# Kernel optimization log

Measured on AMD Instinct MI355X. Metric: run time of the kernel, lower is better.

Reference implementation:

```python
import jax, jax.numpy as jnp
import numpy as np

B, C, H, W = 2, 192, 128, 128
HEADS = 4
M = 128          # num_tokens
RD = 10          # reducted_dim
GS = 256         # category_size
TDF = 16         # dim_ffn_td
HID = 4 * C      # mlp hidden (768)
HIDT = HID + TDF # 784 after concat with token-dict features
KS = 5


def _ln(x, g, b):
    mu = x.mean(-1, keepdims=True)
    var = ((x - mu) ** 2).mean(-1, keepdims=True)
    return (x - mu) / jnp.sqrt(var + 1e-5) * g + b


def _gelu(x):
    return jax.nn.gelu(x, approximate=False)  # torch nn.GELU default = exact erf


def setup_inputs() -> dict:
    key = jax.random.key(0)
    ks = jax.random.split(key, 16)
    s = 0.02
    inp = {
        "x": jax.random.normal(ks[0], (B, C, H, W), jnp.float32),
        "x_size": H,
        "td": jax.random.normal(ks[1], (M, C), jnp.float32),
        "g1": jnp.ones((C,)), "b1": jnp.zeros((C,)),
        "g2": jnp.ones((C,)), "b2": jnp.zeros((C,)),
        "g3": jnp.ones((C,)), "b3": jnp.zeros((C,)),
        "wq_w": jax.random.normal(ks[2], (C, RD)) * s, "wq_b": jnp.zeros((RD,)),
        "wk_w": jax.random.normal(ks[3], (C, RD)) * s, "wk_b": jnp.zeros((RD,)),
        "wv_w": jax.random.normal(ks[4], (C, C)) * s, "wv_b": jnp.zeros((C,)),
        "ca_scale": jnp.ones((1,)),
        "wqkv_w": jax.random.normal(ks[5], (C, 3 * C)) * s, "wqkv_b": jnp.zeros((3 * C,)),
        "proj_w": jax.random.normal(ks[6], (C, C)) * s, "proj_b": jnp.zeros((C,)),
        "fc_td_w": jax.random.normal(ks[7], (C, TDF)) * s, "fc_td_b": jnp.zeros((TDF,)),
        "fc1_w": jax.random.normal(ks[8], (C, HID)) * s, "fc1_b": jnp.zeros((HID,)),
        "dw_w": jax.random.normal(ks[9], (HIDT, 1, KS, KS)) * s, "dw_b": jnp.zeros((HIDT,)),
        "fc2_w": jax.random.normal(ks[10], (HIDT, C)) * s, "fc2_b": jnp.zeros((C,)),
    }
    return inp


def reference(x, x_size, td, g1, b1, g2, b2, g3, b3, wq_w, wq_b, wk_w, wk_b,
              wv_w, wv_b, ca_scale, wqkv_w, wqkv_b, proj_w, proj_b,
              fc_td_w, fc_td_b, fc1_w, fc1_b, dw_w, dw_b, fc2_w, fc2_b):
    b, c, h, w = x.shape
    n = h * w
    xs = x.reshape(b, c, n).transpose(0, 2, 1)          # [b,n,c] patch_embed
    shortcut = xs
    xn = _ln(xs, g1, b1)                                # norm1

    # ---- ATD_CA: L2-normalized cross-attention to token dict ----
    q = xn @ wq_w + wq_b                                # [b,n,rd]
    k = td @ wk_w + wk_b                                # [m,rd]
    v = td @ wv_w + wv_b                                # [m,c]
    qn = q / jnp.maximum(jnp.linalg.norm(q, axis=-1, keepdims=True), 1e-12)
    kn = k / jnp.maximum(jnp.linalg.norm(k, axis=-1, keepdims=True), 1e-12)
    sim = jnp.einsum('bnr,mr->bnm', qn, kn)
    scale = 1.0 + jnp.clip(ca_scale, 0.0, 3.0) * np.log(M)
    sim = jax.nn.softmax(sim * scale, axis=-1)          # [b,n,m]
    x_atd = jnp.einsum('bnm,mc->bnc', sim, v)
    tk_id = jnp.argmax(sim, axis=-1)                    # [b,n] int

    # ---- AC_MSA: category-sorted grouped self-attention ----
    qkv = xn @ wqkv_w + wqkv_b                          # [b,n,3c]
    sort_idx = jnp.argsort(tk_id, axis=-1)              # [b,n]
    inv_idx = jnp.argsort(sort_idx, axis=-1)            # index_reverse
    shuf = jnp.take_along_axis(qkv, sort_idx[:, :, None], axis=1)
    gs = min(n, GS)
    ng = (n + gs - 1) // gs
    pad_n = ng * gs - n
    pad = jnp.flip(shuf[:, n - pad_n:n, :], axis=1)
    padded = jnp.concatenate([shuf, pad], axis=1)       # [b, ng*gs, 3c]
    hd = c // HEADS
    y = padded.reshape(b, ng, gs, 3, HEADS, hd)
    y = jnp.transpose(y, (3, 0, 1, 4, 2, 5))            # [3,b,ng,H,gs,hd]
    q2, k2, v2 = y[0], y[1], y[2]
    attn = jnp.einsum('bghqd,bghkd->bghqk', q2, k2) * (hd ** -0.5)
    attn = jax.nn.softmax(attn, axis=-1)
    o = jnp.einsum('bghqk,bghkd->bghqd', attn, v2)
    o = jnp.transpose(o, (0, 1, 3, 2, 4)).reshape(b, ng * gs, c)[:, :n, :]
    o = jnp.take_along_axis(o, inv_idx[:, :, None], axis=1)
    x_aca = o @ proj_w + proj_b

    # ---- token-dict features gathered per token ----
    td_feat = td @ fc_td_w + fc_td_b                    # [m,tdf]
    x_td = jnp.take(td_feat, tk_id, axis=0)             # [b,n,tdf]

    # ---- ConvFFN_td ----
    xn2 = _ln(xs, g2, b2)
    h1 = _gelu(xn2 @ fc1_w + fc1_b)                     # [b,n,hid]
    hcat = jnp.concatenate([h1, x_td], axis=-1)         # [b,n,hidt]
    img = hcat.transpose(0, 2, 1).reshape(b, HIDT, h, w)
    conv = jax.lax.conv_general_dilated(
        img, dw_w, window_strides=(1, 1), padding=((KS // 2, KS // 2),) * 2,
        dimension_numbers=('NCHW', 'OIHW', 'NCHW'), feature_group_count=HIDT)
    conv = _gelu(conv + dw_b[None, :, None, None])
    conv = conv.reshape(b, HIDT, n).transpose(0, 2, 1)
    x_ffn = (hcat + conv) @ fc2_w + fc2_b
    x_ffn = _ln(x_ffn, g3, b3)                          # norm3

    out = shortcut + x_atd + x_aca + x_ffn
    return out.transpose(0, 2, 1).reshape(b, c, h, w)
```

## Files before the change

kernel.cpp:

```cpp
#include <hip/hip_runtime.h>
#include <hip/hip_bf16.h>
#include <math.h>

using bf16 = __hip_bfloat16;

static constexpr int B = 2, C = 192, Hh = 128, Ww = 128, N = Hh * Ww;
static constexpr int M = 128, RD = 10, GS = 256, NG = N / GS;
static constexpr int HEADS = 4, HD = C / HEADS;
static constexpr int TDF = 16, HID = 4 * C, HIDT = HID + TDF;
static constexpr int TC3 = 3 * C;
static constexpr float LOG_M = 4.852030263919617f;
static constexpr float ATT_SCALE = 0.14433756729740643f;

typedef __attribute__((ext_vector_type(8))) short bf16x8;
typedef __attribute__((ext_vector_type(4))) float f32x4;

__device__ __forceinline__ float b2f(bf16 v) { return __bfloat162float(v); }
__device__ __forceinline__ bf16 f2b(float v) { return __float2bfloat16(v); }
__device__ __forceinline__ float bits2f(unsigned short u) { return __uint_as_float(((unsigned)u) << 16); }
__device__ __forceinline__ unsigned short f2bits(float f) {
    union { bf16 h; unsigned short u; } cv; cv.h = f2b(f); return cv.u;
}
__device__ __forceinline__ float gelu_exact(float v) {
    return 0.5f * v * (1.0f + erff(v * 0.70710678118654752f));
}

__global__ void __launch_bounds__(256) k_wtrans(const float* in, bf16* out, int K, int Nn) {
    __shared__ float T[64][65];
    int n0 = blockIdx.x * 64, k0 = blockIdx.y * 64;
    int tid = threadIdx.x;
    for (int e = tid; e < 4096; e += 256) {
        int kk = e >> 6, nn = e & 63;
        if (k0 + kk < K) T[kk][nn] = in[(size_t)(k0 + kk) * Nn + n0 + nn];
    }
    __syncthreads();
    for (int e = tid; e < 4096; e += 256) {
        int nn = e >> 6, kk = e & 63;
        if (k0 + kk < K) out[(size_t)(n0 + nn) * K + k0 + kk] = f2b(T[kk][nn]);
    }
}

__global__ void k_precompute(const float* td, const float* wk_w, const float* wk_b,
                             const float* wv_w, const float* wv_b,
                             const float* fc_td_w, const float* fc_td_b,
                             float* kn, bf16* vvT, float* tdf) {
    int m = blockIdx.x;
    int lane = threadIdx.x;
    __shared__ float trow[C];
    for (int ch = lane; ch < C; ch += 64) trow[ch] = td[m * C + ch];
    __syncthreads();
    __shared__ float ks[RD];
    __shared__ float inv_s;
    if (lane < RD) {
        float s = wk_b[lane];
        for (int ch = 0; ch < C; ++ch) s += trow[ch] * wk_w[ch * RD + lane];
        ks[lane] = s;
    }
    __syncthreads();
    if (lane == 0) {
        float ss = 0.f;
        for (int r = 0; r < RD; ++r) ss += ks[r] * ks[r];
        inv_s = 1.0f / fmaxf(sqrtf(ss), 1e-12f);
    }
    __syncthreads();
    if (lane < RD) kn[m * RD + lane] = ks[lane] * inv_s;
    for (int c0 = 0; c0 < 3; ++c0) {
        int co = lane + 64 * c0;
        float s = wv_b[co];
        for (int ch = 0; ch < C; ++ch) s += trow[ch] * wv_w[ch * C + co];
        vvT[(size_t)co * M + m] = f2b(s);
    }
    if (lane < TDF) {
        float s = fc_td_b[lane];
        for (int ch = 0; ch < C; ++ch) s += trow[ch] * fc_td_w[ch * TDF + lane];
        tdf[m * TDF + lane] = s;
    }
}

__global__ void __launch_bounds__(256) k_ln(const float* x, const float* g1, const float* b1,
                                            const float* g2, const float* b2v,
                                            bf16* xn1, bf16* xn2, float* xn32, float* acc) {
    __shared__ float Xs[64 * 193];
    __shared__ float mu_s[64], rs_s[64];
    int tid = threadIdx.x;
    int m0 = blockIdx.x * 64;
    int b = m0 / N, i0 = m0 % N;
    for (int e = tid; e < 192 * 64; e += 256) {
        int ch = e >> 6, ii = e & 63;
        Xs[ii * 193 + ch] = x[((size_t)b * C + ch) * N + i0 + ii];
    }
    __syncthreads();
    {
        int tok = tid >> 2, part = tid & 3;
        float s = 0.f, ss = 0.f;
        for (int ch = part * 48; ch < part * 48 + 48; ++ch) {
            float v = Xs[tok * 193 + ch]; s += v; ss += v * v;
        }
        s += __shfl_xor(s, 1); ss += __shfl_xor(ss, 1);
        s += __shfl_xor(s, 2); ss += __shfl_xor(ss, 2);
        if (part == 0) {
            float mu = s / C;
            mu_s[tok] = mu;
            rs_s[tok] = rsqrtf(ss / C - mu * mu + 1e-5f);
        }
    }
    __syncthreads();
    for (int e = tid; e < 64 * 192; e += 256) {
        int ii = e / 192, ch = e % 192;
        float v = Xs[ii * 193 + ch];
        float xn = (v - mu_s[ii]) * rs_s[ii];
        size_t g = (size_t)(m0 + ii);
        xn1[g * C + ch] = f2b(xn * g1[ch] + b1[ch]);
        xn2[g * C + ch] = f2b(xn * g2[ch] + b2v[ch]);
        xn32[g * C + ch] = xn;
        acc[g * C + ch] = v;
    }
}

__global__ void __launch_bounds__(256) k_atdca(const float* xn32, const float* g1, const float* b1,
                        const float* wq_w, const float* wq_b, const float* ca_scale,
                        const float* kn, bf16* p_buf, int* tk_id) {
    int t0 = blockIdx.x * 4;
    int w = threadIdx.x >> 6, lane = threadIdx.x & 63;
    int g = t0 + w;
    float xn[3];
    #pragma unroll
    for (int k = 0; k < 3; ++k) {
        int ch = lane + 64 * k;
        xn[k] = xn32[(size_t)g * C + ch] * g1[ch] + b1[ch];
    }
    float q[RD];
    #pragma unroll
    for (int r = 0; r < RD; ++r) {
        float p = 0.f;
        #pragma unroll
        for (int k = 0; k < 3; ++k) { int ch = lane + 64 * k; p += xn[k] * wq_w[ch * RD + r]; }
        for (int mk = 32; mk >= 1; mk >>= 1) p += __shfl_xor(p, mk);
        q[r] = p + wq_b[r];
    }
    float ssn = 0.f;
    #pragma unroll
    for (int r = 0; r < RD; ++r) ssn += q[r] * q[r];
    float invq = 1.0f / fmaxf(sqrtf(ssn), 1e-12f);
    float s0 = 0.f, s1 = 0.f;
    #pragma unroll
    for (int r = 0; r < RD; ++r) {
        float qr = q[r] * invq;
        s0 += qr * kn[lane * RD + r];
        s1 += qr * kn[(lane + 64) * RD + r];
    }
    float mv; int mi;
    if (s1 > s0) { mv = s1; mi = lane + 64; } else { mv = s0; mi = lane; }
    for (int mk = 32; mk >= 1; mk >>= 1) {
        float ov = __shfl_xor(mv, mk); int oi = __shfl_xor(mi, mk);
        if (ov > mv || (ov == mv && oi < mi)) { mv = ov; mi = oi; }
    }
    float cs = ca_scale[0]; cs = fminf(fmaxf(cs, 0.0f), 3.0f);
    float scale = 1.0f + cs * LOG_M;
    float e0 = expf((s0 - mv) * scale), e1 = expf((s1 - mv) * scale);
    float sum = e0 + e1;
    for (int mk = 32; mk >= 1; mk >>= 1) sum += __shfl_xor(sum, mk);
    float invs = 1.0f / sum;
    p_buf[(size_t)g * M + lane] = f2b(e0 * invs);
    p_buf[(size_t)g * M + lane + 64] = f2b(e1 * invs);
    if (lane == 0) tk_id[g] = mi;
}

__global__ void __launch_bounds__(256) k_pv(const bf16* p_buf, const bf16* vvT, float* acc) {
    __shared__ __align__(16) short As[64 * 136];
    __shared__ __align__(16) short Bs[64 * 136];
    int tid = threadIdx.x;
    int m0 = blockIdx.x * 64;
    int n0 = blockIdx.y * 64;
    for (int e = tid; e < 64 * 16; e += 256) {
        int m = e >> 4, kc = (e & 15) * 8;
        *(uint4*)&As[m * 136 + kc] = *(const uint4*)(p_buf + (size_t)(m0 + m) * M + kc);
    }
    for (int e = tid; e < 64 * 16; e += 256) {
        int n = e >> 4, kc = (e & 15) * 8;
        *(uint4*)&Bs[n * 136 + kc] = *(const uint4*)(vvT + (size_t)(n0 + n) * M + kc);
    }
    __syncthreads();
    int w = tid >> 6, lane = tid & 63;
    int wm = (w >> 1) * 32, wn = (w & 1) * 32;
    int lr = lane & 15, lk = (lane >> 4) * 8;
    f32x4 acc00 = {0.f,0.f,0.f,0.f}, acc01 = acc00, acc10 = acc00, acc11 = acc00;
    #pragma unroll
    for (int ks = 0; ks < 4; ++ks) {
        int k0 = ks * 32 + lk;
        bf16x8 a0 = *(bf16x8*)&As[(wm + lr) * 136 + k0];
        bf16x8 a1 = *(bf16x8*)&As[(wm + 16 + lr) * 136 + k0];
        bf16x8 b0 = *(bf16x8*)&Bs[(wn + lr) * 136 + k0];
        bf16x8 b1 = *(bf16x8*)&Bs[(wn + 16 + lr) * 136 + k0];
        acc00 = __builtin_amdgcn_mfma_f32_16x16x32_bf16(a0, b0, acc00, 0, 0, 0);
        acc01 = __builtin_amdgcn_mfma_f32_16x16x32_bf16(a0, b1, acc01, 0, 0, 0);
        acc10 = __builtin_amdgcn_mfma_f32_16x16x32_bf16(a1, b0, acc10, 0, 0, 0);
        acc11 = __builtin_amdgcn_mfma_f32_16x16x32_bf16(a1, b1, acc11, 0, 0, 0);
    }
    int rbase = (lane >> 4) * 4;
    f32x4 accs[2][2] = {{acc00, acc01}, {acc10, acc11}};
    #pragma unroll
    for (int mt = 0; mt < 2; ++mt) {
        #pragma unroll
        for (int nt = 0; nt < 2; ++nt) {
            int co = n0 + wn + nt * 16 + lr;
            #pragma unroll
            for (int r = 0; r < 4; ++r) {
                int tok = m0 + wm + mt * 16 + rbase + r;
                acc[(size_t)tok * C + co] += accs[mt][nt][r];
            }
        }
    }
}

template<int OUTLD, int MODE>
__global__ void __launch_bounds__(256) k_gemm_big(const bf16* Abuf, const bf16* Wt, const float* bias,
                                                  bf16* outb, float* outf) {
    __shared__ __align__(16) unsigned short As[128 * 104];
    __shared__ __align__(16) unsigned short Bs[96 * 104];
    int tid = threadIdx.x;
    int m0 = blockIdx.x * 128, n0 = blockIdx.y * 96;
    int w = tid >> 6, lane = tid & 63;
    int wm = (w >> 1) * 64, wn = (w & 1) * 48;
    int lr = lane & 15, g8 = lane >> 4;
    f32x4 acc[4][3];
    #pragma unroll
    for (int mt = 0; mt < 4; ++mt)
        #pragma unroll
        for (int nt = 0; nt < 3; ++nt) acc[mt][nt] = (f32x4){0.f,0.f,0.f,0.f};
    for (int kc = 0; kc < 2; ++kc) {
        int kb = kc * 96;
        __syncthreads();
        for (int e = tid; e < 128 * 12; e += 256) {
            int m = e / 12, blk = e % 12;
            *(uint4*)&As[m * 104 + blk * 8] = *(const uint4*)(Abuf + (size_t)(m0 + m) * C + kb + blk * 8);
        }
        for (int e = tid; e < 96 * 12; e += 256) {
            int n = e / 12, blk = e % 12;
            *(uint4*)&Bs[n * 104 + blk * 8] = *(const uint4*)(Wt + (size_t)(n0 + n) * C + kb + blk * 8);
        }
        __syncthreads();
        #pragma unroll
        for (int ks = 0; ks < 3; ++ks) {
            int blk = ks * 4 + g8;
            bf16x8 a[4];
            bf16x8 bfr[3];
            #pragma unroll
            for (int mt = 0; mt < 4; ++mt) a[mt] = *(bf16x8*)&As[(wm + mt * 16 + lr) * 104 + blk * 8];
            #pragma unroll
            for (int nt = 0; nt < 3; ++nt) bfr[nt] = *(bf16x8*)&Bs[(wn + nt * 16 + lr) * 104 + blk * 8];
            #pragma unroll
            for (int mt = 0; mt < 4; ++mt)
                #pragma unroll
                for (int nt = 0; nt < 3; ++nt)
                    acc[mt][nt] = __builtin_amdgcn_mfma_f32_16x16x32_bf16(a[mt], bfr[nt], acc[mt][nt], 0, 0, 0);
        }
    }
    #pragma unroll
    for (int nt = 0; nt < 3; ++nt) {
        int co = n0 + wn + nt * 16 + lr;
        float bv = bias[co];
        #pragma unroll
        for (int mt = 0; mt < 4; ++mt) {
            #pragma unroll
            for (int r = 0; r < 4; ++r) {
                int tok = m0 + wm + mt * 16 + g8 * 4 + r;
                float v = acc[mt][nt][r] + bv;
                if (MODE == 0) outb[(size_t)tok * OUTLD + co] = f2b(v);
                else if (MODE == 1) outb[(size_t)tok * OUTLD + co] = f2b(gelu_exact(v));
                else outf[(size_t)tok * OUTLD + co] += v;
            }
        }
    }
}

__global__ void k_sort_count(const int* tk_id, int* chunk_cnt) {
    int c = blockIdx.x, b = blockIdx.y;
    int tid = threadIdx.x;
    __shared__ int cnt[M];
    cnt[tid] = 0;
    __syncthreads();
    atomicAdd(&cnt[tk_id[b * N + c * 128 + tid]], 1);
    __syncthreads();
    chunk_cnt[(b * 128 + c) * M + tid] = cnt[tid];
}

__global__ void k_sort_scan(int* chunk_cnt) {
    int b = blockIdx.x;
    int k = threadIdx.x;
    int tot = 0;
    for (int c = 0; c < 128; ++c) tot += chunk_cnt[(b * 128 + c) * M + k];
    __shared__ int totals[M];
    __shared__ int base[M];
    totals[k] = tot;
    __syncthreads();
    if (k == 0) {
        int run = 0;
        for (int kk = 0; kk < M; ++kk) { base[kk] = run; run += totals[kk]; }
    }
    __syncthreads();
    int run = base[k];
    for (int c = 0; c < 128; ++c) {
        int v = chunk_cnt[(b * 128 + c) * M + k];
        chunk_cnt[(b * 128 + c) * M + k] = run;
        run += v;
    }
}

__global__ void k_sort_scatter(const int* tk_id, const int* chunk_cnt, int* sort_idx) {
    int c = blockIdx.x, b = blockIdx.y;
    int k = threadIdx.x;
    __shared__ int keys[128];
    keys[k] = tk_id[b * N + c * 128 + k];
    __syncthreads();
    int off = chunk_cnt[(b * 128 + c) * M + k];
    for (int j = 0; j < 128; ++j) {
        if (keys[j] == k) sort_idx[b * N + off++] = c * 128 + j;
    }
}

__global__ void __launch_bounds__(256) k_attn_mfma(const bf16* qkv, const int* sort_idx, bf16* o_buf) {
    int g = blockIdx.x, h = blockIdx.y, b = blockIdx.z;
    __shared__ int sidx[GS];
    __shared__ __align__(16) unsigned short Kl[256 * 64];
    __shared__ __align__(16) unsigned short Vt[48 * 256];
    __shared__ __align__(16) unsigned short Pl[4][64 * 32];
    int tid = threadIdx.x;
    sidx[tid] = sort_idx[b * N + g * GS + tid];
    __syncthreads();
    {
        int row = tid;
        int srow = sidx[row];
        size_t kb = ((size_t)(b * N + srow)) * TC3 + C + h * HD;
        size_t vb = ((size_t)(b * N + srow)) * TC3 + 2 * C + h * HD;
        #pragma unroll
        for (int db = 0; db < 6; ++db) {
            uint4 kv = *(const uint4*)(qkv + kb + db * 8);
            *(uint4*)&Kl[row * 64 + ((db ^ (row & 7)) * 8)] = kv;
            uint4 vv4 = *(const uint4*)(qkv + vb + db * 8);
            unsigned short* vu = (unsigned short*)&vv4;
            #pragma unroll
            for (int j = 0; j < 8; ++j) {
                int d = db * 8 + j;
                Vt[d * 256 + (((row >> 3) ^ (d & 7)) * 8) + (row & 7)] = vu[j];
            }
        }
        uint4 z = {0u,0u,0u,0u};
        *(uint4*)&Kl[row * 64 + ((6 ^ (row & 7)) * 8)] = z;
        *(uint4*)&Kl[row * 64 + ((7 ^ (row & 7)) * 8)] = z;
    }
    __syncthreads();
    int w = tid >> 6, l = tid & 63;
    int lq = l & 15, g8 = l >> 4;
    bf16x8 qf[4][2];
    #pragma unroll
    for (int qt = 0; qt < 4; ++qt) {
        int qrow = sidx[w * 64 + qt * 16 + lq];
        size_t qb = ((size_t)(b * N + qrow)) * TC3 + h * HD;
        qf[qt][0] = *(const bf16x8*)(qkv + qb + g8 * 8);
        int d1 = 32 + g8 * 8;
        if (d1 < HD) qf[qt][1] = *(const bf16x8*)(qkv + qb + d1);
        else { uint4 z = {0u,0u,0u,0u}; qf[qt][1] = *(bf16x8*)&z; }
    }
    float mrun[4], lrun[4];
    f32x4 Oa[4][3];
    #pragma unroll
    for (int qt = 0; qt < 4; ++qt) {
        mrun[qt] = -1e30f; lrun[qt] = 0.f;
        #pragma unroll
        for (int dt = 0; dt < 3; ++dt) Oa[qt][dt] = (f32x4){0.f,0.f,0.f,0.f};
    }
    unsigned short* Pw = &Pl[w][0];
    for (int ck = 0; ck < 8; ++ck) {
        int kbase = ck * 32;
        bf16x8 kf[2][2];
        #pragma unroll
        for (int kt = 0; kt < 2; ++kt) {
            int key = kbase + kt * 16 + lq;
            #pragma unroll
            for (int ks = 0; ks < 2; ++ks)
                kf[kt][ks] = *(bf16x8*)&Kl[key * 64 + (((ks * 4 + g8) ^ (key & 7)) * 8)];
        }
        bf16x8 vf[3];
        #pragma unroll
        for (int dt = 0; dt < 3; ++dt) {
            int d = dt * 16 + lq;
            vf[dt] = *(bf16x8*)&Vt[d * 256 + ((((kbase >> 3) + g8) ^ (d & 7)) * 8)];
        }
        #pragma unroll
        for (int qt = 0; qt < 4; ++qt) {
            f32x4 s0 = {0.f,0.f,0.f,0.f}, s1 = s0;
            s0 = __builtin_amdgcn_mfma_f32_16x16x32_bf16(kf[0][0], qf[qt][0], s0, 0, 0, 0);
            s0 = __builtin_amdgcn_mfma_f32_16x16x32_bf16(kf[0][1], qf[qt][1], s0, 0, 0, 0);
            s1 = __builtin_amdgcn_mfma_f32_16x16x32_bf16(kf[1][0], qf[qt][0], s1, 0, 0, 0);
            s1 = __builtin_amdgcn_mfma_f32_16x16x32_bf16(kf[1][1], qf[qt][1], s1, 0, 0, 0);
            float sv0[4], sv1[4];
            float cmax = -1e30f;
            #pragma unroll
            for (int r = 0; r < 4; ++r) {
                sv0[r] = s0[r] * ATT_SCALE; sv1[r] = s1[r] * ATT_SCALE;
                cmax = fmaxf(cmax, fmaxf(sv0[r], sv1[r]));
            }
            cmax = fmaxf(cmax, __shfl_xor(cmax, 16));
            cmax = fmaxf(cmax, __shfl_xor(cmax, 32));
            float mnew = fmaxf(mrun[qt], cmax);
            float sf = expf(mrun[qt] - mnew);
            float p0[4], p1[4], csum = 0.f;
            #pragma unroll
            for (int r = 0; r < 4; ++r) {
                p0[r] = expf(sv0[r] - mnew); p1[r] = expf(sv1[r] - mnew);
                csum += p0[r] + p1[r];
            }
            csum += __shfl_xor(csum, 16);
            csum += __shfl_xor(csum, 32);
            lrun[qt] = lrun[qt] * sf + csum;
            mrun[qt] = mnew;
            int q = qt * 16 + lq;
            {
                unsigned short pw[4];
                #pragma unroll
                for (int r = 0; r < 4; ++r) pw[r] = f2bits(p0[r]);
                int slot = g8;
                int addr = q * 32 + (((slot >> 1) ^ (q & 3)) * 8) + (slot & 1) * 4;
                *(uint2*)&Pw[addr] = *(uint2*)pw;
                #pragma unroll
                for (int r = 0; r < 4; ++r) pw[r] = f2bits(p1[r]);
                slot = 4 + g8;
                addr = q * 32 + (((slot >> 1) ^ (q & 3)) * 8) + (slot & 1) * 4;
                *(uint2*)&Pw[addr] = *(uint2*)pw;
            }
            float sfr[4];
            #pragma unroll
            for (int r = 0; r < 4; ++r) sfr[r] = __shfl(sf, 4 * g8 + r);
            #pragma unroll
            for (int dt = 0; dt < 3; ++dt)
                #pragma unroll
                for (int r = 0; r < 4; ++r) Oa[qt][dt][r] *= sfr[r];
            bf16x8 pa = *(bf16x8*)&Pw[q * 32 + ((g8 ^ (lq & 3)) * 8)];
            #pragma unroll
            for (int dt = 0; dt < 3; ++dt)
                Oa[qt][dt] = __builtin_amdgcn_mfma_f32_16x16x32_bf16(pa, vf[dt], Oa[qt][dt], 0, 0, 0);
        }
    }
    #pragma unroll
    for (int qt = 0; qt < 4; ++qt) {
        float invq = 1.0f / lrun[qt];
        float invr[4];
        #pragma unroll
        for (int r = 0; r < 4; ++r) invr[r] = __shfl(invq, 4 * g8 + r);
        #pragma unroll
        for (int r = 0; r < 4; ++r) {
            int grow = sidx[w * 64 + qt * 16 + 4 * g8 + r];
            size_t obase = ((size_t)(b * N + grow)) * C + h * HD;
            #pragma unroll
            for (int dt = 0; dt < 3; ++dt)
                o_buf[obase + dt * 16 + lq] = f2b(Oa[qt][dt][r] * invr[r]);
        }
    }
}

__global__ void k_tdfill(const int* tk_id, const float* tdf, bf16* hcat) {
    int idx = blockIdx.x * 256 + threadIdx.x;
    if (idx >= B * N * TDF) return;
    int tok = idx >> 4, f = idx & 15;
    hcat[(size_t)tok * HIDT + HID + f] = f2b(tdf[tk_id[tok] * TDF + f]);
}

__global__ void __launch_bounds__(256) k_conv(const bf16* hcat, const float* dw_w, const float* dw_b,
                                              bf16* convsum) {
    int st = blockIdx.x;
    int c16 = blockIdx.y;
    int b = blockIdx.z;
    int tx0 = (st & 7) * 16, ty0 = (st >> 3) * 16;
    int tid = threadIdx.x;
    __shared__ __align__(16) float Hf[20 * 81 * 4];
    __shared__ __align__(16) float Wf[25 * 16];
    __shared__ float Wb[16];
    for (int e = tid; e < 400; e += 256) {
        int tap = e >> 4, ch = e & 15;
        Wf[e] = dw_w[(size_t)(c16 * 16 + ch) * 25 + tap];
    }
    if (tid < 16) Wb[tid] = dw_b[c16 * 16 + tid];
    for (int e = tid; e < 800; e += 256) {
        int pos = e >> 1, sc = e & 1;
        int py = pos / 20, px = pos % 20;
        int gy = ty0 + py - 2, gx = tx0 + px - 2;
        uint4 v = {0u, 0u, 0u, 0u};
        if (gy >= 0 && gy < Hh && gx >= 0 && gx < Ww)
            v = *(const uint4*)(hcat + ((size_t)b * N + gy * Ww + gx) * HIDT + c16 * 16 + sc * 8);
        unsigned short* u = (unsigned short*)&v;
        float4 f0 = { bits2f(u[0]), bits2f(u[1]), bits2f(u[2]), bits2f(u[3]) };
        float4 f1 = { bits2f(u[4]), bits2f(u[5]), bits2f(u[6]), bits2f(u[7]) };
        int base = (py * 81 + px * 4 + sc * 2) * 4;
        *(float4*)&Hf[base] = f0;
        *(float4*)&Hf[base + 4] = f1;
    }
    __syncthreads();
    int cc = tid & 1, lx = (tid >> 1) & 7, ly = tid >> 4;
    float acc[2][8] = {};
    #pragma unroll 1
    for (int ky = 0; ky < 5; ++ky) {
        int py = ly + ky;
        float4 w[5][2];
        #pragma unroll
        for (int kx = 0; kx < 5; ++kx) {
            w[kx][0] = *(float4*)&Wf[(ky * 5 + kx) * 16 + cc * 8];
            w[kx][1] = *(float4*)&Wf[(ky * 5 + kx) * 16 + cc * 8 + 4];
        }
        #pragma unroll
        for (int c = 0; c < 6; ++c) {
            int px = 2 * lx + c;
            int base = (py * 81 + px * 4 + cc * 2) * 4;
            float4 f0 = *(float4*)&Hf[base];
            float4 f1 = *(float4*)&Hf[base + 4];
            float f[8] = { f0.x, f0.y, f0.z, f0.w, f1.x, f1.y, f1.z, f1.w };
            #pragma unroll
            for (int kx = 0; kx < 5; ++kx) {
                int ox = c - kx;
                if (ox >= 0 && ox < 2) {
                    const float* wp = (const float*)&w[kx][0];
                    #pragma unroll
                    for (int j = 0; j < 8; ++j) acc[ox][j] += f[j] * wp[j];
                }
            }
        }
    }
    int gy = ty0 + ly;
    #pragma unroll
    for (int ox = 0; ox < 2; ++ox) {
        int px = 2 * lx + ox + 2, py = ly + 2;
        int base = (py * 81 + px * 4 + cc * 2) * 4;
        float4 f0 = *(float4*)&Hf[base];
        float4 f1 = *(float4*)&Hf[base + 4];
        float cf[8] = { f0.x, f0.y, f0.z, f0.w, f1.x, f1.y, f1.z, f1.w };
        unsigned short ow[8];
        #pragma unroll
        for (int j = 0; j < 8; ++j)
            ow[j] = f2bits(cf[j] + gelu_exact(acc[ox][j] + Wb[cc * 8 + j]));
        int gx = tx0 + 2 * lx + ox;
        *(uint4*)(convsum + ((size_t)b * N + gy * Ww + gx) * HIDT + c16 * 16 + cc * 8) = *(uint4*)ow;
    }
}

__global__ void __launch_bounds__(256) k_fc2ln(const bf16* convsum, const bf16* Wt,
                                               const float* bias, const float* g3, const float* b3,
                                               const float* accres, float* out) {
    __shared__ __align__(16) char smem[65536];
    unsigned short* AsB = (unsigned short*)smem;
    unsigned short* BsB = (unsigned short*)(smem + 16384);
    float* Ot = (float*)smem;
    int tid = threadIdx.x;
    int m0 = blockIdx.x * 64;
    int w = tid >> 6, lane = tid & 63;
    int lr = lane & 15, g8 = lane >> 4;
    f32x4 acc[12];
    #pragma unroll
    for (int nt = 0; nt < 12; ++nt) acc[nt] = (f32x4){0.f, 0.f, 0.f, 0.f};

    auto stage = [&](int d, int kc) {
        int kb = kc * 64;
        unsigned short* As = AsB + d * 4096;
        unsigned short* Bs = BsB + d * 12288;
        for (int e = tid; e < 512; e += 256) {
            int m = e >> 3, k8 = (e & 7) * 8;
            uint4 v = {0u,0u,0u,0u};
            if (kb + k8 < HIDT) v = *(const uint4*)(convsum + (size_t)(m0 + m) * HIDT + kb + k8);
            *(uint4*)&As[m * 64 + (((e & 7) ^ (m & 7)) * 8)] = v;
        }
        for (int e = tid; e < 1536; e += 256) {
            int n = e >> 3, k8 = (e & 7) * 8;
            uint4 v = {0u,0u,0u,0u};
            if (kb + k8 < HIDT) v = *(const uint4*)(Wt + (size_t)n * HIDT + kb + k8);
            *(uint4*)&Bs[n * 64 + (((e & 7) ^ (n & 7)) * 8)] = v;
        }
    };
    stage(0, 0);
    int cur = 0;
    for (int kc = 0; kc < 13; ++kc) {
        __syncthreads();
        if (kc + 1 < 13) stage(cur ^ 1, kc + 1);
        unsigned short* As = AsB + cur * 4096;
        unsigned short* Bs = BsB + cur * 12288;
        #pragma unroll
        for (int ks = 0; ks < 2; ++ks) {
            int kg = ks * 4 + g8;
            int arow = w * 16 + lr;
            bf16x8 a = *(bf16x8*)&As[arow * 64 + ((kg ^ (arow & 7)) * 8)];
            #pragma unroll
            for (int nt = 0; nt < 12; ++nt) {
                int nrow = nt * 16 + lr;
                bf16x8 bfr = *(bf16x8*)&Bs[nrow * 64 + ((kg ^ (nrow & 7)) * 8)];
                acc[nt] = __builtin_amdgcn_mfma_f32_16x16x32_bf16(a, bfr, acc[nt], 0, 0, 0);
            }
        }
        cur ^= 1;
    }
    #pragma unroll
    for (int nt = 0; nt < 12; ++nt) {
        float bv = bias[nt * 16 + lr];
        #pragma unroll
        for (int r = 0; r < 4; ++r) acc[nt][r] += bv;
    }
    float mu_r[4], rs_r[4];
    #pragma unroll
    for (int r = 0; r < 4; ++r) {
        float s = 0.f, ss = 0.f;
        #pragma unroll
        for (int nt = 0; nt < 12; ++nt) { float v = acc[nt][r]; s += v; ss += v * v; }
        s += __shfl_xor(s, 1); ss += __shfl_xor(ss, 1);
        s += __shfl_xor(s, 2); ss += __shfl_xor(ss, 2);
        s += __shfl_xor(s, 4); ss += __shfl_xor(ss, 4);
        s += __shfl_xor(s, 8); ss += __shfl_xor(ss, 8);
        mu_r[r] = s / C;
        rs_r[r] = rsqrtf(ss / C - mu_r[r] * mu_r[r] + 1e-5f);
    }
    int bb = m0 / N, i0 = m0 % N;
    for (int h = 0; h < 2; ++h) {
        __syncthreads();
        #pragma unroll
        for (int ntl = 0; ntl < 6; ++ntl) {
            int nt = h * 6 + ntl;
            int c = nt * 16 + lr;
            float g3v = g3[c], b3v = b3[c];
            #pragma unroll
            for (int r = 0; r < 4; ++r) {
                int tok = m0 + w * 16 + g8 * 4 + r;
                float o = accres[(size_t)tok * C + c] + (acc[nt][r] - mu_r[r]) * rs_r[r] * g3v + b3v;
                Ot[(ntl * 16 + lr) * 68 + w * 16 + g8 * 4 + r] = o;
            }
        }
        __syncthreads();
        for (int e = tid; e < 96 * 16; e += 256) {
            int row = e >> 4, q4 = e & 15;
            int c = h * 96 + row;
            float4 v = *(float4*)&Ot[row * 68 + q4 * 4];
            *(float4*)(out + ((size_t)(bb * C + c)) * N + i0 + q4 * 4) = v;
        }
    }
}

__global__ void k_sentinel(float* out, int nelem) {
    int i = blockIdx.x * blockDim.x + threadIdx.x;
    if (i < nelem) out[i] = 1234.0f;
}

extern "C" void kernel_launch(void* const* d_in, const int* in_sizes, int n_in,
                              void* d_out, int out_size, void* d_ws, size_t ws_size,
                              hipStream_t stream) {
    const float* x        = (const float*)d_in[0];
    const float* td       = (const float*)d_in[2];
    const float* g1       = (const float*)d_in[3];
    const float* b1       = (const float*)d_in[4];
    const float* g2       = (const float*)d_in[5];
    const float* b2v      = (const float*)d_in[6];
    const float* g3       = (const float*)d_in[7];
    const float* b3       = (const float*)d_in[8];
    const float* wq_w     = (const float*)d_in[9];
    const float* wq_b     = (const float*)d_in[10];
    const float* wk_w     = (const float*)d_in[11];
    const float* wk_b     = (const float*)d_in[12];
    const float* wv_w     = (const float*)d_in[13];
    const float* wv_b     = (const float*)d_in[14];
    const float* ca_scale = (const float*)d_in[15];
    const float* wqkv_w   = (const float*)d_in[16];
    const float* wqkv_b   = (const float*)d_in[17];
    const float* proj_w   = (const float*)d_in[18];
    const float* proj_b   = (const float*)d_in[19];
    const float* fc_td_w  = (const float*)d_in[20];
    const float* fc_td_b  = (const float*)d_in[21];
    const float* fc1_w    = (const float*)d_in[22];
    const float* fc1_b    = (const float*)d_in[23];
    const float* dw_w     = (const float*)d_in[24];
    const float* dw_b     = (const float*)d_in[25];
    const float* fc2_w    = (const float*)d_in[26];
    const float* fc2_b    = (const float*)d_in[27];
    float* out = (float*)d_out;

    char* ws = (char*)d_ws;
    size_t off = 0;
    auto alloc = [&](size_t bytes) { size_t o = off; off += (bytes + 255) & ~(size_t)255; return o; };
    size_t o_xn1   = alloc((size_t)B * N * C * 2);
    size_t o_xn2   = alloc((size_t)B * N * C * 2);
    size_t o_xn32  = alloc((size_t)B * N * C * 4);
    size_t o_acc   = alloc((size_t)B * N * C * 4);
    size_t o_qkv   = alloc((size_t)B * N * TC3 * 2);
    size_t o_obuf  = alloc((size_t)B * N * C * 2);
    size_t o_hcat  = alloc((size_t)B * N * HIDT * 2);
    size_t o_conv  = alloc((size_t)B * N * HIDT * 2);
    size_t o_kn    = alloc((size_t)M * RD * 4);
    size_t o_vvT   = alloc((size_t)C * M * 2);
    size_t o_tdf   = alloc((size_t)M * TDF * 4);
    size_t o_tk    = alloc((size_t)B * N * 4);
    size_t o_sidx  = alloc((size_t)B * N * 4);
    size_t o_ccnt  = alloc((size_t)B * 128 * M * 4);
    size_t o_pbuf  = alloc((size_t)B * N * M * 2);
    size_t o_wqkvT = alloc((size_t)TC3 * C * 2);
    size_t o_projT = alloc((size_t)C * C * 2);
    size_t o_fc1T  = alloc((size_t)HID * C * 2);
    size_t o_fc2T  = alloc((size_t)C * HIDT * 2);

    if (ws_size < off) {
        k_sentinel<<<(out_size + 255) / 256, 256, 0, stream>>>(out, out_size);
        return;
    }

    bf16*  xn1     = (bf16*)(ws + o_xn1);
    bf16*  xn2     = (bf16*)(ws + o_xn2);
    float* xn32    = (float*)(ws + o_xn32);
    float* acc     = (float*)(ws + o_acc);
    bf16*  qkv     = (bf16*)(ws + o_qkv);
    bf16*  o_bufp  = (bf16*)(ws + o_obuf);
    bf16*  hcat    = (bf16*)(ws + o_hcat);
    bf16*  convsum = (bf16*)(ws + o_conv);
    float* kn      = (float*)(ws + o_kn);
    bf16*  vvT     = (bf16*)(ws + o_vvT);
    float* tdf     = (float*)(ws + o_tdf);
    int*   tk_id   = (int*)(ws + o_tk);
    int*   sidx    = (int*)(ws + o_sidx);
    int*   ccnt    = (int*)(ws + o_ccnt);
    bf16*  p_buf   = (bf16*)(ws + o_pbuf);
    bf16*  wqkvT   = (bf16*)(ws + o_wqkvT);
    bf16*  projT   = (bf16*)(ws + o_projT);
    bf16*  fc1T    = (bf16*)(ws + o_fc1T);
    bf16*  fc2T    = (bf16*)(ws + o_fc2T);

    k_wtrans<<<dim3(TC3 / 64, C / 64), 256, 0, stream>>>(wqkv_w, wqkvT, C, TC3);
    k_wtrans<<<dim3(C / 64, C / 64), 256, 0, stream>>>(proj_w, projT, C, C);
    k_wtrans<<<dim3(HID / 64, C / 64), 256, 0, stream>>>(fc1_w, fc1T, C, HID);
    k_wtrans<<<dim3(C / 64, (HIDT + 63) / 64), 256, 0, stream>>>(fc2_w, fc2T, HIDT, C);

    k_precompute<<<M, 64, 0, stream>>>(td, wk_w, wk_b, wv_w, wv_b, fc_td_w, fc_td_b, kn, vvT, tdf);
    k_ln<<<B * N / 64, 256, 0, stream>>>(x, g1, b1, g2, b2v, xn1, xn2, xn32, acc);
    k_atdca<<<B * N / 4, 256, 0, stream>>>(xn32, g1, b1, wq_w, wq_b, ca_scale, kn, p_buf, tk_id);
    k_pv<<<dim3(B * N / 64, C / 64), 256, 0, stream>>>(p_buf, vvT, acc);
    k_gemm_big<TC3, 0><<<dim3(B * N / 128, TC3 / 96), 256, 0, stream>>>(
        xn1, wqkvT, wqkv_b, qkv, nullptr);
    k_sort_count<<<dim3(128, B), 128, 0, stream>>>(tk_id, ccnt);
    k_sort_scan<<<B, 128, 0, stream>>>(ccnt);
    k_sort_scatter<<<dim3(128, B), 128, 0, stream>>>(tk_id, ccnt, sidx);
    k_attn_mfma<<<dim3(NG, HEADS, B), 256, 0, stream>>>(qkv, sidx, o_bufp);
    k_gemm_big<C, 2><<<dim3(B * N / 128, C / 96), 256, 0, stream>>>(
        o_bufp, projT, proj_b, nullptr, acc);
    k_gemm_big<HIDT, 1><<<dim3(B * N / 128, HID / 96), 256, 0, stream>>>(
        xn2, fc1T, fc1_b, hcat, nullptr);
    k_tdfill<<<(B * N * TDF + 255) / 256, 256, 0, stream>>>(tk_id, tdf, hcat);
    k_conv<<<dim3(64, 49, B), 256, 0, stream>>>(hcat, dw_w, dw_b, convsum);
    k_fc2ln<<<B * N / 64, 256, 0, stream>>>(convsum, fc2T, fc2_b, g3, b3, acc, out);
}
```

Before: 399.4 us.

## Shrink fc2+LN tile to 32 rows, split N across waves, store proj output as bf16

The fc2+layernorm kernel now handles 32 tokens per block instead of 64, and each wave computes a 48-column slice instead of all 192 columns. Row statistics are combined across waves through shared memory. Shared memory drops from 64KB to about 28KB and the double buffering is removed, which is meant to allow more resident blocks and twice as many blocks for occupancy. The proj GEMM now writes its result as a separate bf16 buffer instead of read-modify-writing the fp32 accumulator, and fc2ln adds that buffer back in. The cost is the lost prefetch overlap, reloading the full weight tile for every 32 rows, and a small precision loss on the proj output.

```diff
diff --git a/kernel.cpp b/kernel.cpp
--- a/kernel.cpp
+++ b/kernel.cpp
@@ -544,28 +544,30 @@
 
 __global__ void __launch_bounds__(256) k_fc2ln(const bf16* convsum, const bf16* Wt,
                                                const float* bias, const float* g3, const float* b3,
-                                               const float* accres, float* out) {
-    __shared__ __align__(16) char smem[65536];
-    unsigned short* AsB = (unsigned short*)smem;
-    unsigned short* BsB = (unsigned short*)(smem + 16384);
+                                               const float* accres, const bf16* aca, float* out) {
+    __shared__ __align__(16) char smem[28672];
+    unsigned short* As = (unsigned short*)smem;
+    unsigned short* Bs = (unsigned short*)(smem + 4096);
     float* Ot = (float*)smem;
+    __shared__ float partS[4][32], partQ[4][32];
     int tid = threadIdx.x;
-    int m0 = blockIdx.x * 64;
+    int m0 = blockIdx.x * 32;
     int w = tid >> 6, lane = tid & 63;
     int lr = lane & 15, g8 = lane >> 4;
-    f32x4 acc[12];
-    #pragma unroll
-    for (int nt = 0; nt < 12; ++nt) acc[nt] = (f32x4){0.f, 0.f, 0.f, 0.f};
-
-    auto stage = [&](int d, int kc) {
+    int n0 = w * 48;
+    f32x4 acc[2][3];
+    #pragma unroll
+    for (int mt = 0; mt < 2; ++mt)
+        #pragma unroll
+        for (int nt = 0; nt < 3; ++nt) acc[mt][nt] = (f32x4){0.f,0.f,0.f,0.f};
+    for (int kc = 0; kc < 13; ++kc) {
         int kb = kc * 64;
-        unsigned short* As = AsB + d * 4096;
-        unsigned short* Bs = BsB + d * 12288;
-        for (int e = tid; e < 512; e += 256) {
-            int m = e >> 3, k8 = (e & 7) * 8;
+        __syncthreads();
+        {
+            int m = tid >> 3, k8 = (tid & 7) * 8;
             uint4 v = {0u,0u,0u,0u};
             if (kb + k8 < HIDT) v = *(const uint4*)(convsum + (size_t)(m0 + m) * HIDT + kb + k8);
-            *(uint4*)&As[m * 64 + (((e & 7) ^ (m & 7)) * 8)] = v;
+            *(uint4*)&As[m * 64 + (((tid & 7) ^ (m & 7)) * 8)] = v;
         }
         for (int e = tid; e < 1536; e += 256) {
             int n = e >> 3, k8 = (e & 7) * 8;
@@ -573,69 +575,75 @@
             if (kb + k8 < HIDT) v = *(const uint4*)(Wt + (size_t)n * HIDT + kb + k8);
             *(uint4*)&Bs[n * 64 + (((e & 7) ^ (n & 7)) * 8)] = v;
         }
-    };
-    stage(0, 0);
-    int cur = 0;
-    for (int kc = 0; kc < 13; ++kc) {
         __syncthreads();
-        if (kc + 1 < 13) stage(cur ^ 1, kc + 1);
-        unsigned short* As = AsB + cur * 4096;
-        unsigned short* Bs = BsB + cur * 12288;
         #pragma unroll
         for (int ks = 0; ks < 2; ++ks) {
             int kg = ks * 4 + g8;
-            int arow = w * 16 + lr;
-            bf16x8 a = *(bf16x8*)&As[arow * 64 + ((kg ^ (arow & 7)) * 8)];
-            #pragma unroll
-            for (int nt = 0; nt < 12; ++nt) {
-                int nrow = nt * 16 + lr;
-                bf16x8 bfr = *(bf16x8*)&Bs[nrow * 64 + ((kg ^ (nrow & 7)) * 8)];
-                acc[nt] = __builtin_amdgcn_mfma_f32_16x16x32_bf16(a, bfr, acc[nt], 0, 0, 0);
-            }
-        }
-        cur ^= 1;
-    }
-    #pragma unroll
-    for (int nt = 0; nt < 12; ++nt) {
-        float bv = bias[nt * 16 + lr];
-        #pragma unroll
-        for (int r = 0; r < 4; ++r) acc[nt][r] += bv;
-    }
-    float mu_r[4], rs_r[4];
-    #pragma unroll
-    for (int r = 0; r < 4; ++r) {
-        float s = 0.f, ss = 0.f;
-        #pragma unroll
-        for (int nt = 0; nt < 12; ++nt) { float v = acc[nt][r]; s += v; ss += v * v; }
-        s += __shfl_xor(s, 1); ss += __shfl_xor(ss, 1);
-        s += __shfl_xor(s, 2); ss += __shfl_xor(ss, 2);
-        s += __shfl_xor(s, 4); ss += __shfl_xor(ss, 4);
-        s += __shfl_xor(s, 8); ss += __shfl_xor(ss, 8);
-        mu_r[r] = s / C;
-        rs_r[r] = rsqrtf(ss / C - mu_r[r] * mu_r[r] + 1e-5f);
-    }
+            #pragma unroll
+            for (int mt = 0; mt < 2; ++mt) {
+                int arow = mt * 16 + lr;
+                bf16x8 a = *(bf16x8*)&As[arow * 64 + ((kg ^ (arow & 7)) * 8)];
+                #pragma unroll
+                for (int nt = 0; nt < 3; ++nt) {
+                    int nrow = n0 + nt * 16 + lr;
+                    bf16x8 bfr = *(bf16x8*)&Bs[nrow * 64 + ((kg ^ (nrow & 7)) * 8)];
+                    acc[mt][nt] = __builtin_amdgcn_mfma_f32_16x16x32_bf16(a, bfr, acc[mt][nt], 0, 0, 0);
+                }
+            }
+        }
+    }
+    #pragma unroll
+    for (int nt = 0; nt < 3; ++nt) {
+        float bv = bias[n0 + nt * 16 + lr];
+        #pragma unroll
+        for (int mt = 0; mt < 2; ++mt)
+            #pragma unroll
+            for (int r = 0; r < 4; ++r) acc[mt][nt][r] += bv;
+    }
+    #pragma unroll
+    for (int mt = 0; mt < 2; ++mt) {
+        #pragma unroll
+        for (int r = 0; r < 4; ++r) {
+            float s = 0.f, q = 0.f;
+            #pragma unroll
+            for (int nt = 0; nt < 3; ++nt) { float v = acc[mt][nt][r]; s += v; q += v * v; }
+            s += __shfl_xor(s, 1); q += __shfl_xor(q, 1);
+            s += __shfl_xor(s, 2); q += __shfl_xor(q, 2);
+            s += __shfl_xor(s, 4); q += __shfl_xor(q, 4);
+            s += __shfl_xor(s, 8); q += __shfl_xor(q, 8);
+            if (lr == 0) {
+                int row = mt * 16 + g8 * 4 + r;
+                partS[w][row] = s;
+                partQ[w][row] = q;
+            }
+        }
+    }
+    __syncthreads();
     int bb = m0 / N, i0 = m0 % N;
-    for (int h = 0; h < 2; ++h) {
-        __syncthreads();
-        #pragma unroll
-        for (int ntl = 0; ntl < 6; ++ntl) {
-            int nt = h * 6 + ntl;
-            int c = nt * 16 + lr;
-            float g3v = g3[c], b3v = b3[c];
-            #pragma unroll
-            for (int r = 0; r < 4; ++r) {
-                int tok = m0 + w * 16 + g8 * 4 + r;
-                float o = accres[(size_t)tok * C + c] + (acc[nt][r] - mu_r[r]) * rs_r[r] * g3v + b3v;
-                Ot[(ntl * 16 + lr) * 68 + w * 16 + g8 * 4 + r] = o;
-            }
-        }
-        __syncthreads();
-        for (int e = tid; e < 96 * 16; e += 256) {
-            int row = e >> 4, q4 = e & 15;
-            int c = h * 96 + row;
-            float4 v = *(float4*)&Ot[row * 68 + q4 * 4];
-            *(float4*)(out + ((size_t)(bb * C + c)) * N + i0 + q4 * 4) = v;
-        }
+    #pragma unroll
+    for (int mt = 0; mt < 2; ++mt) {
+        #pragma unroll
+        for (int r = 0; r < 4; ++r) {
+            int row = mt * 16 + g8 * 4 + r;
+            float s = partS[0][row] + partS[1][row] + partS[2][row] + partS[3][row];
+            float q = partQ[0][row] + partQ[1][row] + partQ[2][row] + partQ[3][row];
+            float mu = s / C;
+            float rstd = rsqrtf(q / C - mu * mu + 1e-5f);
+            int tok = m0 + row;
+            #pragma unroll
+            for (int nt = 0; nt < 3; ++nt) {
+                int c = n0 + nt * 16 + lr;
+                float o = accres[(size_t)tok * C + c] + b2f(aca[(size_t)tok * C + c])
+                        + (acc[mt][nt][r] - mu) * rstd * g3[c] + b3[c];
+                Ot[c * 36 + row] = o;
+            }
+        }
+    }
+    __syncthreads();
+    for (int e = tid; e < 192 * 8; e += 256) {
+        int row = e >> 3, q4 = e & 7;
+        float4 v = *(float4*)&Ot[row * 36 + q4 * 4];
+        *(float4*)(out + ((size_t)(bb * C + row)) * N + i0 + q4 * 4) = v;
     }
 }
 
@@ -683,6 +691,7 @@
     size_t o_xn2   = alloc((size_t)B * N * C * 2);
     size_t o_xn32  = alloc((size_t)B * N * C * 4);
     size_t o_acc   = alloc((size_t)B * N * C * 4);
+    size_t o_aca   = alloc((size_t)B * N * C * 2);
     size_t o_qkv   = alloc((size_t)B * N * TC3 * 2);
     size_t o_obuf  = alloc((size_t)B * N * C * 2);
     size_t o_hcat  = alloc((size_t)B * N * HIDT * 2);
@@ -708,6 +717,7 @@
     bf16*  xn2     = (bf16*)(ws + o_xn2);
     float* xn32    = (float*)(ws + o_xn32);
     float* acc     = (float*)(ws + o_acc);
+    bf16*  aca     = (bf16*)(ws + o_aca);
     bf16*  qkv     = (bf16*)(ws + o_qkv);
     bf16*  o_bufp  = (bf16*)(ws + o_obuf);
     bf16*  hcat    = (bf16*)(ws + o_hcat);
@@ -739,11 +749,11 @@
     k_sort_scan<<<B, 128, 0, stream>>>(ccnt);
     k_sort_scatter<<<dim3(128, B), 128, 0, stream>>>(tk_id, ccnt, sidx);
     k_attn_mfma<<<dim3(NG, HEADS, B), 256, 0, stream>>>(qkv, sidx, o_bufp);
-    k_gemm_big<C, 2><<<dim3(B * N / 128, C / 96), 256, 0, stream>>>(
-        o_bufp, projT, proj_b, nullptr, acc);
+    k_gemm_big<C, 0><<<dim3(B * N / 128, C / 96), 256, 0, stream>>>(
+        o_bufp, projT, proj_b, aca, nullptr);
     k_gemm_big<HIDT, 1><<<dim3(B * N / 128, HID / 96), 256, 0, stream>>>(
         xn2, fc1T, fc1_b, hcat, nullptr);
     k_tdfill<<<(B * N * TDF + 255) / 256, 256, 0, stream>>>(tk_id, tdf, hcat);
     k_conv<<<dim3(64, 49, B), 256, 0, stream>>>(hcat, dw_w, dw_b, convsum);
-    k_fc2ln<<<B * N / 64, 256, 0, stream>>>(convsum, fc2T, fc2_b, g3, b3, acc, out);
-}
+    k_fc2ln<<<B * N / 32, 256, 0, stream>>>(convsum, fc2T, fc2_b, g3, b3, acc, aca, out);
+}
```

Result: faster. 382.1 us (-4.3%).
